# Kernel optimization log

Hardware: AMD Instinct MI355X
Metric: run time of the kernel (lower is better)

## Reference

```python
import jax, jax.numpy as jnp
import numpy as np

SCALE_BASE = 512.0
GN_EPS = 1e-5


def _xpos(x, downscale):
    # x: [..., L, D]; XPOS rotary embedding with exponential length scale (torchscale)
    L, D = x.shape[-2], x.shape[-1]
    half = D // 2
    base = (jnp.arange(0, D, 2, dtype=jnp.float32) + 0.4 * D) / (1.4 * D)  # [half]
    min_pos = -(L // 2)
    power = (jnp.arange(min_pos, min_pos + L, dtype=jnp.float32) / SCALE_BASE)[:, None]
    scale = base[None, :] ** power  # [L, half]
    inv_freq = 1.0 / (10000.0 ** (jnp.arange(half, dtype=jnp.float32) / half))
    ang = jnp.arange(L, dtype=jnp.float32)[:, None] * inv_freq[None, :]  # [L, half]
    sin, cos = jnp.sin(ang), jnp.cos(ang)
    if downscale:
        scale = 1.0 / scale
    sin_s = jnp.repeat(sin * scale, 2, axis=-1)  # duplicate_interleave -> [L, D]
    cos_s = jnp.repeat(cos * scale, 2, axis=-1)
    x1, x2 = x[..., ::2], x[..., 1::2]
    rot = jnp.stack((-x2, x1), axis=-1).reshape(x.shape)  # rotate_every_two
    return x * cos_s + rot * sin_s


def _decay_mask(L, H):
    gammas = 1.0 - jnp.exp(jnp.linspace(np.log(1.0 / 32.0), np.log(1.0 / 512.0), H)).astype(jnp.float32)
    idx = jnp.arange(L)
    dist = idx[:, None] - idx[None, :]  # [L, L]
    causal = dist >= 0
    d = jnp.maximum(dist, 0).astype(jnp.float32)
    # gamma^|n-s| below diagonal, 0 above (gamma^inf = 0 in the torch version)
    return jnp.where(causal[None], gammas[:, None, None] ** d[None], 0.0)  # [H, L, L]


def setup_inputs() -> dict:
    key = jax.random.key(0)
    ks = jax.random.split(key, 9)
    B, L, D, H = 2, 2048, 1024, 16
    hd = D // H
    return {
        "query": jax.random.normal(ks[0], (B, L, D), jnp.float32),
        "key": jax.random.normal(ks[1], (B, L, D), jnp.float32),
        "value": jax.random.normal(ks[2], (B, L, D), jnp.float32),
        "W_Q": jax.random.normal(ks[3], (H, D, hd), jnp.float32) / D,
        "W_K": jax.random.normal(ks[4], (H, D, hd), jnp.float32) / D,
        "W_V": jax.random.normal(ks[5], (H, D, hd), jnp.float32) / D,
        "g_w": jax.random.normal(ks[6], (D, D), jnp.float32) * (2.0 / (D + D)) ** 0.5,
        "g_b": jnp.zeros((D,), jnp.float32),
        "out_w": jax.random.normal(ks[7], (D, D), jnp.float32) * (2.0 / (D + D)) ** 0.5,
        "out_b": jnp.zeros((D,), jnp.float32),
    }


def reference(query, key, value, W_Q, W_K, W_V, g_w, g_b, out_w, out_b):
    B, L, D = query.shape
    H = W_Q.shape[0]
    q = jnp.einsum('bld,hde->bhle', query, W_Q)
    k = jnp.einsum('bld,hde->bhle', key, W_K)
    v = jnp.einsum('bld,hde->bhle', value, W_V)
    q = _xpos(q, downscale=False)
    k = _xpos(k, downscale=True)
    # retention_parallel: QK^T * decay mask (no softmax, no scale), then @ V
    sim = jnp.einsum('bhnd,bhsd->bhns', q, k) * _decay_mask(L, H)[None]
    ret = jnp.einsum('bhns,bhsd->bhnd', sim, v)  # [B, H, L, hd]
    # GroupNorm(num_groups=H, affine=False) on (b n, h d): normalize per (b, h, n) over hd
    mu = ret.mean(axis=-1, keepdims=True)
    var = ret.var(axis=-1, keepdims=True)
    ret = (ret - mu) / jnp.sqrt(var + GN_EPS)
    ret = ret.transpose(0, 2, 1, 3).reshape(B, L, D)  # b h n d -> b n (h d)
    gate = jax.nn.silu(query @ g_w.T + g_b)
    return (ret * gate) @ out_w.T + out_b
```

## Files before the change

### kernel.cpp

```cpp
#include <hip/hip_runtime.h>
#include <cstdint>

#define B_  2
#define L_  2048
#define D_  1024
#define H_  16
#define HD_ 64
#define M_  (B_*L_)

#define MD  4194304u
#define DD  1048576u

#define OFF_XQB  0u
#define OFF_XKB  (MD)
#define OFF_XVB  (2u*MD)
#define OFF_WQTH (3u*MD)
#define OFF_WKTH (3u*MD + DD)
#define OFF_WVTH (3u*MD + 2u*DD)
#define OFF_GWH  (3u*MD + 3u*DD)
#define OFF_OWH  (3u*MD + 4u*DD)
#define OFF_GATE (3u*MD + 5u*DD)
#define OFF_QB2  (OFF_GATE + MD)
#define OFF_KB2  (OFF_GATE + 2u*MD)
#define OFF_VTG  (OFF_GATE + 3u*MD)
#define OFF_F32  (OFF_GATE + 4u*MD)
#define OFF_ABUF OFF_XQB

typedef __attribute__((ext_vector_type(8))) short bf16x8;
typedef __attribute__((ext_vector_type(8))) unsigned short u16x8;
typedef __attribute__((ext_vector_type(4))) short s16x4;
typedef __attribute__((ext_vector_type(4))) float f32x4;

__device__ __forceinline__ unsigned short f2b(float x){
  union { float f; unsigned u; } a; a.f = x;
  unsigned r = a.u + 0x7FFFu + ((a.u >> 16) & 1u);
  return (unsigned short)(r >> 16);
}
__device__ __forceinline__ float b2f(unsigned short u){
  union { unsigned u; float f; } a; a.u = ((unsigned)u) << 16; return a.f;
}

__global__ __launch_bounds__(256) void prep_kernel(
    const float* __restrict__ q, const float* __restrict__ k,
    const float* __restrict__ v, const float* __restrict__ gw,
    const float* __restrict__ ow, const float* __restrict__ WQ,
    const float* __restrict__ WK, const float* __restrict__ WV,
    unsigned short* __restrict__ ws)
{
  __shared__ float t[32][33];
  const int bx = blockIdx.x, tid = threadIdx.x;
  if (bx < 12288) {
    size_t i = ((size_t)bx * 256 + tid) * 4;
    const float* src; unsigned short* dst;
    if (i < MD)         { src = q + i;           dst = ws + OFF_XQB + i; }
    else if (i < 2u*MD) { src = k + (i - MD);    dst = ws + OFF_XKB + (i - MD); }
    else                { src = v + (i - 2u*MD); dst = ws + OFF_XVB + (i - 2u*MD); }
    float4 vv = *(const float4*)src;
    ushort4 o;
    o.x = f2b(vv.x); o.y = f2b(vv.y); o.z = f2b(vv.z); o.w = f2b(vv.w);
    *(ushort4*)dst = o;
  } else if (bx < 14336) {
    size_t i = ((size_t)(bx - 12288) * 256 + tid) * 4;
    const float* src; unsigned short* dh;
    if (i < DD) { src = gw + i; dh = ws + OFF_GWH + i; }
    else        { src = ow + (i - DD); dh = ws + OFF_OWH + (i - DD); }
    float4 vv = *(const float4*)src;
    ushort4 o;
    o.x = f2b(vv.x); o.y = f2b(vv.y); o.z = f2b(vv.z); o.w = f2b(vv.w);
    *(ushort4*)dh = o;
  } else if (bx < 17408) {
    const int tb = bx - 14336;
    const int w = tb >> 10;
    const int tb2 = tb & 1023;
    const int hh = tb2 >> 6, tt = tb2 & 63;
    const int e0 = (tt & 1) * 32, d0 = (tt >> 1) * 32;
    const float* in = (w == 0) ? WQ : (w == 1) ? WK : WV;
    unsigned short* outH = ws + ((w == 0) ? OFF_WQTH : (w == 1) ? OFF_WKTH : OFF_WVTH);
    const int x = tid & 31, y0 = tid >> 5;
    for (int yy = y0; yy < 32; yy += 8)
      t[yy][x] = in[((size_t)hh * D_ + d0 + yy) * HD_ + e0 + x];
    __syncthreads();
    for (int yy = y0; yy < 32; yy += 8) {
      const size_t o = ((size_t)hh * HD_ + e0 + yy) * D_ + d0 + x;
      outH[o] = f2b(t[x][yy]);
    }
  } else {
    float* fb = (float*)(ws + OFF_F32);
    const int idx = (bx - 17408) * 256 + tid;
    const int l = idx >> 5, i = idx & 31;
    const double base = (2.0 * (double)i + 25.6) / 89.6;
    const double p = ((double)l - 1024.0) / 512.0;
    const double sc = exp2(p * log2(base));
    const double invf = exp2(-(double)i * (13.287712379549449 / 32.0));
    const double ang = (double)l * invf;
    const double s = sin(ang), c = cos(ang);
    fb[          l * 32 + i] = (float)(c * sc);
    fb[ 65536 +  l * 32 + i] = (float)(s * sc);
    fb[131072 +  l * 32 + i] = (float)(c / sc);
    fb[196608 +  l * 32 + i] = (float)(s / sc);
  }
}

__device__ __forceinline__ void gemm_body(
    const unsigned short* __restrict__ Ah,
    const unsigned short* __restrict__ Bh,
    float* __restrict__ outF, unsigned short* __restrict__ outB,
    const float* __restrict__ ct, const float* __restrict__ st,
    const float* __restrict__ bias, int mode, int ldc, int M0, int N0,
    char* Ash, char* Bsh)
{
  const int tid = threadIdx.x;
  const int wave = tid >> 6, lane = tid & 63;
  const int wm = wave & 1, wn = wave >> 1;
  const int mlane = lane & 15, kgrp = lane >> 4;
  const int rl = lane >> 3, csel = lane & 7;
  const char* Abh = (const char*)Ah;
  const char* Bbh = (const char*)Bh;

  f32x4 acc[4][2] = {};

  for (int K0 = 0; K0 < 1024; K0 += 64) {
    __syncthreads();
#pragma unroll
    for (int t = 0; t < 4; ++t) {
      const int row = wave * 32 + t * 8 + rl;
      const int gc = csel ^ (row & 7);
      const size_t gofs = ((size_t)(M0 + row) * 1024 + K0) * 2 + gc * 16;
      const int off = (wave * 32 + t * 8) * 128 + lane * 16;
      __builtin_amdgcn_global_load_lds(
          (const __attribute__((address_space(1))) void*)(Abh + gofs),
          (__attribute__((address_space(3))) void*)(Ash + off), 16, 0, 0);
    }
#pragma unroll
    for (int t = 0; t < 2; ++t) {
      const int row = wave * 16 + t * 8 + rl;
      const int gc = csel ^ (row & 7);
      const size_t gofs = ((size_t)(N0 + row) * 1024 + K0) * 2 + gc * 16;
      const int off = (wave * 16 + t * 8) * 128 + lane * 16;
      __builtin_amdgcn_global_load_lds(
          (const __attribute__((address_space(1))) void*)(Bbh + gofs),
          (__attribute__((address_space(3))) void*)(Bsh + off), 16, 0, 0);
    }
    __syncthreads();
#pragma unroll
    for (int kh = 0; kh < 2; ++kh) {
      bf16x8 afh[4], bfh[2];
#pragma unroll
      for (int tm = 0; tm < 4; ++tm) {
        const int r = wm * 64 + tm * 16 + mlane;
        afh[tm] = *(const bf16x8*)(Ash + r * 128 + (((kh * 4 + kgrp) ^ (r & 7)) << 4));
      }
#pragma unroll
      for (int tn = 0; tn < 2; ++tn) {
        const int r = wn * 32 + tn * 16 + mlane;
        bfh[tn] = *(const bf16x8*)(Bsh + r * 128 + (((kh * 4 + kgrp) ^ (r & 7)) << 4));
      }
#pragma unroll
      for (int tm = 0; tm < 4; ++tm)
#pragma unroll
        for (int tn = 0; tn < 2; ++tn)
          acc[tm][tn] = __builtin_amdgcn_mfma_f32_16x16x32_bf16(afh[tm], bfh[tn], acc[tm][tn], 0, 0, 0);
    }
  }

#pragma unroll
  for (int tm = 0; tm < 4; ++tm)
#pragma unroll
    for (int tn = 0; tn < 2; ++tn) {
      f32x4 v = acc[tm][tn];
#pragma unroll
      for (int r = 0; r < 4; ++r) {
        const int grow = M0 + wm * 64 + tm * 16 + (lane >> 4) * 4 + r;
        const int gcol = N0 + wn * 32 + tn * 16 + mlane;
        float val = v[r];
        if (mode == 1 || mode == 2) {
          const float partner = __shfl_xor(val, 1);
          const int l = grow & (L_ - 1);
          const int i = (gcol >> 1) & 31;
          const float c = ct[l * 32 + i], s = st[l * 32 + i];
          val = (gcol & 1) ? (val * c + partner * s) : (val * c - partner * s);
          outB[(size_t)grow * ldc + gcol] = f2b(val);
        } else if (mode == 0) {
          outB[(size_t)grow * ldc + gcol] = f2b(val);
        } else if (mode == 3) {
          const float x = val + bias[gcol];
          outB[(size_t)grow * ldc + gcol] = f2b(x / (1.0f + expf(-x)));
        } else {
          outF[(size_t)grow * ldc + gcol] = val + bias[gcol];
        }
      }
    }
}

__global__ __launch_bounds__(256) void gemm4_kernel(
    unsigned short* __restrict__ ws, const float* __restrict__ g_b)
{
  __shared__ __align__(16) char Ash[128 * 128];
  __shared__ __align__(16) char Bsh[64 * 128];
  const int z = blockIdx.y, bx = blockIdx.x;
  float* fb = (float*)(ws + OFF_F32);
  if (z == 0) {
    gemm_body(ws + OFF_XQB, ws + OFF_WQTH, nullptr, ws + OFF_QB2,
              fb, fb + 65536, nullptr,
              1, D_, (bx & 31) * 128, (bx >> 5) * 64, Ash, Bsh);
  } else if (z == 1) {
    gemm_body(ws + OFF_XKB, ws + OFF_WKTH, nullptr, ws + OFF_KB2,
              fb + 131072, fb + 196608, nullptr,
              2, D_, (bx & 31) * 128, (bx >> 5) * 64, Ash, Bsh);
  } else if (z == 2) {
    gemm_body(ws + OFF_WVTH, ws + OFF_XVB, nullptr, ws + OFF_VTG,
              nullptr, nullptr, nullptr,
              0, M_, (bx & 7) * 128, (bx >> 3) * 64, Ash, Bsh);
  } else {
    gemm_body(ws + OFF_XQB, ws + OFF_GWH, nullptr, ws + OFF_GATE,
              nullptr, nullptr, g_b,
              3, D_, (bx & 31) * 128, (bx >> 5) * 64, Ash, Bsh);
  }
}

__global__ __launch_bounds__(256) void gemm_final_kernel(
    unsigned short* __restrict__ ws, const float* __restrict__ out_b,
    float* __restrict__ out)
{
  __shared__ __align__(16) char Ash[128 * 128];
  __shared__ __align__(16) char Bsh[64 * 128];
  gemm_body(ws + OFF_ABUF, ws + OFF_OWH,
            out, nullptr, nullptr, nullptr, out_b,
            4, D_, blockIdx.x * 128, blockIdx.y * 64, Ash, Bsh);
}

#define AQ_OFF  0
#define AK_OFF  8192
#define AV_OFF  24576

__global__ __launch_bounds__(256, 4) void attn_mfma_kernel(
    const unsigned short* __restrict__ qg, const unsigned short* __restrict__ kg,
    const unsigned short* __restrict__ vtg, const unsigned short* __restrict__ gate,
    unsigned short* __restrict__ Abuf)
{
  __shared__ __align__(16) char smem[40960];
  const int tid = threadIdx.x, wave = tid >> 6, lane = tid & 63;
  const int mlane = lane & 15, kgrp = lane >> 4;
  const int rl8 = lane >> 3, cs8 = lane & 7;
  const int rl4 = lane >> 4, cs16 = lane & 15;

  const int id = blockIdx.x;
  const int bh = id & 31;
  const int xq = 31 - (id >> 5);
  const int b = bh >> 4, h = bh & 15;
  const int l0 = xq * 64;

  const double gamma_d = 1.0 - exp(-3.4657359027997265 + (double)h * (-0.18483924814931873));
  const double lg2g_d  = log2(gamma_d);
  const float lg2g = (float)lg2g_d;
  float gmrf[4];
#pragma unroll
  for (int r = 0; r < 4; ++r) gmrf[r] = (float)exp2(-(double)r * lg2g_d);

#pragma unroll
  for (int t = 0; t < 2; ++t) {
    const int row = 16 * wave + 8 * t + rl8;
    const char* g = (const char*)(qg + (size_t)(b * L_ + l0 + row) * D_ + h * HD_ + ((cs8 ^ (row & 7)) << 3));
    __builtin_amdgcn_global_load_lds(
        (const __attribute__((address_space(1))) void*)g,
        (__attribute__((address_space(3))) void*)(smem + AQ_OFF + (16 * wave + 8 * t) * 128 + lane * 16),
        16, 0, 0);
  }
  __syncthreads();

  bf16x8 qa[2];
  {
    const int row = 16 * wave + mlane;
#pragma unroll
    for (int kk = 0; kk < 2; ++kk)
      qa[kk] = *(const bf16x8*)(smem + AQ_OFF + row * 128 + (((4 * kk + kgrp) ^ (row & 7)) << 4));
  }
  const int nrow = l0 + 16 * wave + mlane;
  const int prow = 16 * wave + mlane;

  f32x4 racc[4] = {};
  const int nst = (xq + 2) >> 1;

  for (int it = 0; it < nst; ++it) {
    const int s0 = it * 128;
    __syncthreads();
#pragma unroll
    for (int t = 0; t < 4; ++t) {
      const int row = 32 * wave + 8 * t + rl8;
      const char* gk = (const char*)(kg + (size_t)(b * L_ + s0 + row) * D_ + h * HD_ + ((cs8 ^ (row & 7)) << 3));
      __builtin_amdgcn_global_load_lds(
          (const __attribute__((address_space(1))) void*)gk,
          (__attribute__((address_space(3))) void*)(smem + AK_OFF + (32 * wave + 8 * t) * 128 + lane * 16),
          16, 0, 0);
    }
#pragma unroll
    for (int t = 0; t < 4; ++t) {
      const int row = 16 * wave + 4 * t + rl4;
      const char* gv = (const char*)(vtg + (size_t)(h * HD_ + row) * M_ + b * L_ + s0 + ((cs16 ^ (row & 7)) << 3));
      __builtin_amdgcn_global_load_lds(
          (const __attribute__((address_space(1))) void*)gv,
          (__attribute__((address_space(3))) void*)(smem + AV_OFF + (16 * wave + 4 * t) * 256 + lane * 16),
          16, 0, 0);
    }
    __syncthreads();

    f32x4 sf[8];
#pragma unroll
    for (int tn = 0; tn < 8; ++tn) {
      const int row = 16 * tn + mlane;
      const bf16x8 kb0 = *(const bf16x8*)(smem + AK_OFF + row * 128 + ((kgrp ^ (row & 7)) << 4));
      const bf16x8 kb1 = *(const bf16x8*)(smem + AK_OFF + row * 128 + (((4 + kgrp) ^ (row & 7)) << 4));
      f32x4 z = {};
      z = __builtin_amdgcn_mfma_f32_16x16x32_bf16(kb0, qa[0], z, 0, 0, 0);
      sf[tn] = __builtin_amdgcn_mfma_f32_16x16x32_bf16(kb1, qa[1], z, 0, 0, 0);
    }

    __syncthreads();

    const bool needMask = (it == nst - 1);
#pragma unroll
    for (int tn = 0; tn < 8; ++tn) {
      const int dd = nrow - (s0 + 16 * tn + 4 * kgrp);
      const float wbase = exp2f((float)dd * lg2g);
      float vv[4];
#pragma unroll
      for (int r = 0; r < 4; ++r) {
        float w = wbase * gmrf[r];
        if (needMask) w = (dd - r >= 0) ? w : 0.0f;
        vv[r] = sf[tn][r] * w;
      }
      s16x4 pk;
      pk[0] = (short)f2b(vv[0]); pk[1] = (short)f2b(vv[1]);
      pk[2] = (short)f2b(vv[2]); pk[3] = (short)f2b(vv[3]);
      *(s16x4*)(smem + AK_OFF + prow * 256 +
                (((2 * tn + (kgrp >> 1)) ^ (prow & 7)) << 4) + ((kgrp & 1) << 3)) = pk;
    }
    asm volatile("s_waitcnt lgkmcnt(0)" ::: "memory");

    bf16x8 pa[4];
#pragma unroll
    for (int kk = 0; kk < 4; ++kk)
      pa[kk] = *(const bf16x8*)(smem + AK_OFF + prow * 256 + (((4 * kk + kgrp) ^ (prow & 7)) << 4));
#pragma unroll
    for (int te = 0; te < 4; ++te) {
      const int rowE = 16 * te + mlane;
#pragma unroll
      for (int kk = 0; kk < 4; ++kk) {
        const bf16x8 vbf = *(const bf16x8*)(smem + AV_OFF + rowE * 256 + (((4 * kk + kgrp) ^ (rowE & 7)) << 4));
        racc[te] = __builtin_amdgcn_mfma_f32_16x16x32_bf16(pa[kk], vbf, racc[te], 0, 0, 0);
      }
    }
  }

#pragma unroll
  for (int r = 0; r < 4; ++r) {
    float vv[4], sm = 0.0f, sq = 0.0f;
#pragma unroll
    for (int tn = 0; tn < 4; ++tn) {
      vv[tn] = racc[tn][r];
      sm += vv[tn]; sq += vv[tn] * vv[tn];
    }
#pragma unroll
    for (int off = 1; off < 16; off <<= 1) {
      sm += __shfl_xor(sm, off);
      sq += __shfl_xor(sq, off);
    }
    const float mu = sm * (1.0f / 64.0f);
    float var = sq * (1.0f / 64.0f) - mu * mu;
    var = fmaxf(var, 0.0f);
    const float inv = 1.0f / sqrtf(var + 1e-5f);
    const int row = l0 + 16 * wave + kgrp * 4 + r;
    const size_t base = (size_t)(b * L_ + row) * D_ + h * HD_;
#pragma unroll
    for (int tn = 0; tn < 4; ++tn) {
      const int c = 16 * tn + mlane;
      const float g = b2f(gate[base + c]);
      Abuf[base + c] = f2b((vv[tn] - mu) * inv * g);
    }
  }
}

extern "C" void kernel_launch(void* const* d_in, const int* in_sizes, int n_in,
                              void* d_out, int out_size, void* d_ws, size_t ws_size,
                              hipStream_t stream)
{
  const float* query = (const float*)d_in[0];
  const float* key   = (const float*)d_in[1];
  const float* value = (const float*)d_in[2];
  const float* W_Q   = (const float*)d_in[3];
  const float* W_K   = (const float*)d_in[4];
  const float* W_V   = (const float*)d_in[5];
  const float* g_w   = (const float*)d_in[6];
  const float* g_b   = (const float*)d_in[7];
  const float* out_w = (const float*)d_in[8];
  const float* out_b = (const float*)d_in[9];
  float* out = (float*)d_out;

  unsigned short* ws = (unsigned short*)d_ws;

  prep_kernel<<<17664, 256, 0, stream>>>(query, key, value, g_w, out_w,
                                         W_Q, W_K, W_V, ws);

  gemm4_kernel<<<dim3(512, 4), 256, 0, stream>>>(ws, g_b);

  attn_mfma_kernel<<<1024, 256, 0, stream>>>(ws + OFF_QB2, ws + OFF_KB2,
                                             ws + OFF_VTG, ws + OFF_GATE,
                                             ws + OFF_ABUF);

  gemm_final_kernel<<<dim3(32, 16), 256, 0, stream>>>(ws, out_b, out);
}
```

Measured before the change: 236.2 us.

## Enlarge GEMM tiles to 128x128, reorder attention blocks, streamline decay weighting

```diff
diff --git a/kernel.cpp b/kernel.cpp
--- a/kernel.cpp
+++ b/kernel.cpp
@@ -27,7 +27,6 @@
 #define OFF_ABUF OFF_XQB
 
 typedef __attribute__((ext_vector_type(8))) short bf16x8;
-typedef __attribute__((ext_vector_type(8))) unsigned short u16x8;
 typedef __attribute__((ext_vector_type(4))) short s16x4;
 typedef __attribute__((ext_vector_type(4))) float f32x4;
 
@@ -117,7 +116,7 @@
   const char* Abh = (const char*)Ah;
   const char* Bbh = (const char*)Bh;
 
-  f32x4 acc[4][2] = {};
+  f32x4 acc[4][4] = {};
 
   for (int K0 = 0; K0 < 1024; K0 += 64) {
     __syncthreads();
@@ -132,11 +131,11 @@
           (__attribute__((address_space(3))) void*)(Ash + off), 16, 0, 0);
     }
 #pragma unroll
-    for (int t = 0; t < 2; ++t) {
-      const int row = wave * 16 + t * 8 + rl;
+    for (int t = 0; t < 4; ++t) {
+      const int row = wave * 32 + t * 8 + rl;
       const int gc = csel ^ (row & 7);
       const size_t gofs = ((size_t)(N0 + row) * 1024 + K0) * 2 + gc * 16;
-      const int off = (wave * 16 + t * 8) * 128 + lane * 16;
+      const int off = (wave * 32 + t * 8) * 128 + lane * 16;
       __builtin_amdgcn_global_load_lds(
           (const __attribute__((address_space(1))) void*)(Bbh + gofs),
           (__attribute__((address_space(3))) void*)(Bsh + off), 16, 0, 0);
@@ -144,21 +143,21 @@
     __syncthreads();
 #pragma unroll
     for (int kh = 0; kh < 2; ++kh) {
-      bf16x8 afh[4], bfh[2];
+      bf16x8 afh[4], bfh[4];
 #pragma unroll
       for (int tm = 0; tm < 4; ++tm) {
         const int r = wm * 64 + tm * 16 + mlane;
         afh[tm] = *(const bf16x8*)(Ash + r * 128 + (((kh * 4 + kgrp) ^ (r & 7)) << 4));
       }
 #pragma unroll
-      for (int tn = 0; tn < 2; ++tn) {
-        const int r = wn * 32 + tn * 16 + mlane;
+      for (int tn = 0; tn < 4; ++tn) {
+        const int r = wn * 64 + tn * 16 + mlane;
         bfh[tn] = *(const bf16x8*)(Bsh + r * 128 + (((kh * 4 + kgrp) ^ (r & 7)) << 4));
       }
 #pragma unroll
       for (int tm = 0; tm < 4; ++tm)
 #pragma unroll
-        for (int tn = 0; tn < 2; ++tn)
+        for (int tn = 0; tn < 4; ++tn)
           acc[tm][tn] = __builtin_amdgcn_mfma_f32_16x16x32_bf16(afh[tm], bfh[tn], acc[tm][tn], 0, 0, 0);
     }
   }
@@ -166,12 +165,12 @@
 #pragma unroll
   for (int tm = 0; tm < 4; ++tm)
 #pragma unroll
-    for (int tn = 0; tn < 2; ++tn) {
+    for (int tn = 0; tn < 4; ++tn) {
       f32x4 v = acc[tm][tn];
 #pragma unroll
       for (int r = 0; r < 4; ++r) {
         const int grow = M0 + wm * 64 + tm * 16 + (lane >> 4) * 4 + r;
-        const int gcol = N0 + wn * 32 + tn * 16 + mlane;
+        const int gcol = N0 + wn * 64 + tn * 16 + mlane;
         float val = v[r];
         if (mode == 1 || mode == 2) {
           const float partner = __shfl_xor(val, 1);
@@ -196,25 +195,25 @@
     unsigned short* __restrict__ ws, const float* __restrict__ g_b)
 {
   __shared__ __align__(16) char Ash[128 * 128];
-  __shared__ __align__(16) char Bsh[64 * 128];
+  __shared__ __align__(16) char Bsh[128 * 128];
   const int z = blockIdx.y, bx = blockIdx.x;
   float* fb = (float*)(ws + OFF_F32);
   if (z == 0) {
     gemm_body(ws + OFF_XQB, ws + OFF_WQTH, nullptr, ws + OFF_QB2,
               fb, fb + 65536, nullptr,
-              1, D_, (bx & 31) * 128, (bx >> 5) * 64, Ash, Bsh);
+              1, D_, (bx & 31) * 128, (bx >> 5) * 128, Ash, Bsh);
   } else if (z == 1) {
     gemm_body(ws + OFF_XKB, ws + OFF_WKTH, nullptr, ws + OFF_KB2,
               fb + 131072, fb + 196608, nullptr,
-              2, D_, (bx & 31) * 128, (bx >> 5) * 64, Ash, Bsh);
+              2, D_, (bx & 31) * 128, (bx >> 5) * 128, Ash, Bsh);
   } else if (z == 2) {
     gemm_body(ws + OFF_WVTH, ws + OFF_XVB, nullptr, ws + OFF_VTG,
               nullptr, nullptr, nullptr,
-              0, M_, (bx & 7) * 128, (bx >> 3) * 64, Ash, Bsh);
+              0, M_, (bx & 7) * 128, (bx >> 3) * 128, Ash, Bsh);
   } else {
     gemm_body(ws + OFF_XQB, ws + OFF_GWH, nullptr, ws + OFF_GATE,
               nullptr, nullptr, g_b,
-              3, D_, (bx & 31) * 128, (bx >> 5) * 64, Ash, Bsh);
+              3, D_, (bx & 31) * 128, (bx >> 5) * 128, Ash, Bsh);
   }
 }
 
@@ -223,10 +222,10 @@
     float* __restrict__ out)
 {
   __shared__ __align__(16) char Ash[128 * 128];
-  __shared__ __align__(16) char Bsh[64 * 128];
+  __shared__ __align__(16) char Bsh[128 * 128];
   gemm_body(ws + OFF_ABUF, ws + OFF_OWH,
             out, nullptr, nullptr, nullptr, out_b,
-            4, D_, blockIdx.x * 128, blockIdx.y * 64, Ash, Bsh);
+            4, D_, blockIdx.x * 128, blockIdx.y * 128, Ash, Bsh);
 }
 
 #define AQ_OFF  0
@@ -246,13 +245,15 @@
 
   const int id = blockIdx.x;
   const int bh = id & 31;
-  const int xq = 31 - (id >> 5);
+  const int g = id >> 5;
+  const int xq = (g < 16) ? (31 - g) : (g - 16);
   const int b = bh >> 4, h = bh & 15;
   const int l0 = xq * 64;
 
   const double gamma_d = 1.0 - exp(-3.4657359027997265 + (double)h * (-0.18483924814931873));
   const double lg2g_d  = log2(gamma_d);
   const float lg2g = (float)lg2g_d;
+  const float g16 = (float)exp2(-16.0 * lg2g_d);
   float gmrf[4];
 #pragma unroll
   for (int r = 0; r < 4; ++r) gmrf[r] = (float)exp2(-(double)r * lg2g_d);
@@ -260,9 +261,9 @@
 #pragma unroll
   for (int t = 0; t < 2; ++t) {
     const int row = 16 * wave + 8 * t + rl8;
-    const char* g = (const char*)(qg + (size_t)(b * L_ + l0 + row) * D_ + h * HD_ + ((cs8 ^ (row & 7)) << 3));
+    const char* gq = (const char*)(qg + (size_t)(b * L_ + l0 + row) * D_ + h * HD_ + ((cs8 ^ (row & 7)) << 3));
     __builtin_amdgcn_global_load_lds(
-        (const __attribute__((address_space(1))) void*)g,
+        (const __attribute__((address_space(1))) void*)gq,
         (__attribute__((address_space(3))) void*)(smem + AQ_OFF + (16 * wave + 8 * t) * 128 + lane * 16),
         16, 0, 0);
   }
@@ -317,23 +318,37 @@
 
     __syncthreads();
 
-    const bool needMask = (it == nst - 1);
-#pragma unroll
-    for (int tn = 0; tn < 8; ++tn) {
-      const int dd = nrow - (s0 + 16 * tn + 4 * kgrp);
-      const float wbase = exp2f((float)dd * lg2g);
-      float vv[4];
-#pragma unroll
-      for (int r = 0; r < 4; ++r) {
-        float w = wbase * gmrf[r];
-        if (needMask) w = (dd - r >= 0) ? w : 0.0f;
-        vv[r] = sf[tn][r] * w;
-      }
-      s16x4 pk;
-      pk[0] = (short)f2b(vv[0]); pk[1] = (short)f2b(vv[1]);
-      pk[2] = (short)f2b(vv[2]); pk[3] = (short)f2b(vv[3]);
-      *(s16x4*)(smem + AK_OFF + prow * 256 +
-                (((2 * tn + (kgrp >> 1)) ^ (prow & 7)) << 4) + ((kgrp & 1) << 3)) = pk;
+    float wbase = exp2f((float)(nrow - s0 - 4 * kgrp) * lg2g);
+    if (it != nst - 1) {
+#pragma unroll
+      for (int tn = 0; tn < 8; ++tn) {
+        float vv[4];
+#pragma unroll
+        for (int r = 0; r < 4; ++r)
+          vv[r] = sf[tn][r] * (wbase * gmrf[r]);
+        uint2 pk;
+        asm("v_cvt_pk_bf16_f32 %0, %1, %2" : "=v"(pk.x) : "v"(vv[0]), "v"(vv[1]));
+        asm("v_cvt_pk_bf16_f32 %0, %1, %2" : "=v"(pk.y) : "v"(vv[2]), "v"(vv[3]));
+        *(uint2*)(smem + AK_OFF + prow * 256 +
+                  (((2 * tn + (kgrp >> 1)) ^ (prow & 7)) << 4) + ((kgrp & 1) << 3)) = pk;
+        wbase *= g16;
+      }
+    } else {
+      const int dd0 = nrow - s0 - 4 * kgrp;
+#pragma unroll
+      for (int tn = 0; tn < 8; ++tn) {
+        const int dd = dd0 - 16 * tn;
+        float vv[4];
+#pragma unroll
+        for (int r = 0; r < 4; ++r)
+          vv[r] = (dd >= r) ? sf[tn][r] * (wbase * gmrf[r]) : 0.0f;
+        uint2 pk;
+        asm("v_cvt_pk_bf16_f32 %0, %1, %2" : "=v"(pk.x) : "v"(vv[0]), "v"(vv[1]));
+        asm("v_cvt_pk_bf16_f32 %0, %1, %2" : "=v"(pk.y) : "v"(vv[2]), "v"(vv[3]));
+        *(uint2*)(smem + AK_OFF + prow * 256 +
+                  (((2 * tn + (kgrp >> 1)) ^ (prow & 7)) << 4) + ((kgrp & 1) << 3)) = pk;
+        wbase *= g16;
+      }
     }
     asm volatile("s_waitcnt lgkmcnt(0)" ::: "memory");
 
@@ -374,8 +389,8 @@
 #pragma unroll
     for (int tn = 0; tn < 4; ++tn) {
       const int c = 16 * tn + mlane;
-      const float g = b2f(gate[base + c]);
-      Abuf[base + c] = f2b((vv[tn] - mu) * inv * g);
+      const float gt = b2f(gate[base + c]);
+      Abuf[base + c] = f2b((vv[tn] - mu) * inv * gt);
     }
   }
 }
@@ -401,11 +416,11 @@
   prep_kernel<<<17664, 256, 0, stream>>>(query, key, value, g_w, out_w,
                                          W_Q, W_K, W_V, ws);
 
-  gemm4_kernel<<<dim3(512, 4), 256, 0, stream>>>(ws, g_b);
+  gemm4_kernel<<<dim3(256, 4), 256, 0, stream>>>(ws, g_b);
 
   attn_mfma_kernel<<<1024, 256, 0, stream>>>(ws + OFF_QB2, ws + OFF_KB2,
                                              ws + OFF_VTG, ws + OFF_GATE,
                                              ws + OFF_ABUF);
 
-  gemm_final_kernel<<<dim3(32, 16), 256, 0, stream>>>(ws, out_b, out);
-}
+  gemm_final_kernel<<<dim3(32, 8), 256, 0, stream>>>(ws, out_b, out);
+}
```

Measured after the change: 236.6 us. No clear change (+0.2%).
